# Performance work log

Measured on AMD Instinct MI355X. Metric: run time of the kernel, lower is better.

## Reference

```python
import jax, jax.numpy as jnp
import numpy as np

N_SRC = 50000
N_DST = 50000
N_EDGES = 1_600_000
D_IN = 128
D_OUT = 128
NUM_HEADS = 8
SCALE = float((D_OUT // NUM_HEADS) ** 0.5)


def setup_inputs() -> dict:
    key = jax.random.key(0)
    ks = jax.random.split(key, 10)
    s = 1.0 / np.sqrt(D_IN)
    return {
        "src_feat": jax.random.normal(ks[0], (N_SRC, D_IN), dtype=jnp.float32),
        "dst_feat": jax.random.normal(ks[1], (N_DST, D_OUT), dtype=jnp.float32),
        "src_idx": jax.random.randint(ks[2], (N_EDGES,), 0, N_SRC, dtype=jnp.int64),
        "dst_idx": jax.random.randint(ks[3], (N_EDGES,), 0, N_DST, dtype=jnp.int64),
        "Wq": jax.random.normal(ks[4], (D_OUT, D_OUT), dtype=jnp.float32) * s,
        "bq": jnp.zeros((D_OUT,), dtype=jnp.float32),
        "Wk": jax.random.normal(ks[5], (D_OUT, D_IN), dtype=jnp.float32) * s,
        "bk": jnp.zeros((D_OUT,), dtype=jnp.float32),
        "Wv": jax.random.normal(ks[6], (D_OUT, D_IN), dtype=jnp.float32) * s,
        "bv": jnp.zeros((D_OUT,), dtype=jnp.float32),
    }


def reference(src_feat, dst_feat, src_idx, dst_idx, Wq, bq, Wk, bk, Wv, bv):
    # Node-level projections (torch Linear: x @ W.T + b)
    Q = dst_feat @ Wq.T + bq            # [N_dst, D_OUT]
    K = src_feat @ Wk.T + bk            # [N_src, D_OUT]
    V = src_feat @ Wv.T + bv            # [N_src, D_OUT]

    # Edge-wise full-dim dot-product score (heads only affect the scale)
    score = jnp.sum(Q[dst_idx] * K[src_idx], axis=-1) / SCALE  # [E]

    # Segment softmax over incoming edges of each destination node
    m = jax.ops.segment_max(score, dst_idx, num_segments=N_DST)   # [N_dst]
    e = jnp.exp(score - m[dst_idx])                               # [E]
    denom = jax.ops.segment_sum(e, dst_idx, num_segments=N_DST)   # [N_dst]
    attn = e / denom[dst_idx]                                     # [E]

    # Weighted V scatter-sum to destination nodes
    out = jax.ops.segment_sum(attn[:, None] * V[src_idx], dst_idx,
                              num_segments=N_DST)                 # [N_dst, D_OUT]
    return out
```

## Files before the change

kernel.cpp:

```cpp
#include <hip/hip_runtime.h>
#include <hip/hip_bf16.h>


#define D 128
#define INV_SCALE 0.25f
#define E1 4096
#define BCAP 10240

typedef __attribute__((ext_vector_type(8))) short bf16x8;
typedef __attribute__((ext_vector_type(4))) float f32x4;
typedef __attribute__((ext_vector_type(4))) int v4i;
typedef __attribute__((ext_vector_type(4))) unsigned v4u;

static __device__ __forceinline__ unsigned short f2bf(float f) {
  unsigned u = __float_as_uint(f);
  u += 0x7fff + ((u >> 16) & 1);
  return (unsigned short)(u >> 16);
}
static __device__ __forceinline__ float bfl(unsigned u) {
  return __uint_as_float(u << 16);
}
static __device__ __forceinline__ float bfh(unsigned u) {
  return __uint_as_float(u & 0xffff0000u);
}

__global__ __launch_bounds__(256) void cvt_w_kernel(
    const float* __restrict__ Wq, const float* __restrict__ Wk,
    const float* __restrict__ Wv, unsigned short* __restrict__ oq,
    unsigned short* __restrict__ ok, unsigned short* __restrict__ ov, int n) {
  int i = blockIdx.x * 256 + threadIdx.x;
  if (i < n) {
    oq[i] = f2bf(Wq[i]);
    ok[i] = f2bf(Wk[i]);
    ov[i] = f2bf(Wv[i]);
  }
}

__global__ __launch_bounds__(256) void gemm_q_kernel(
    const float* __restrict__ X, const unsigned short* __restrict__ Wb,
    const float* __restrict__ bias, float* __restrict__ out, int N) {
  const int lane = threadIdx.x & 63;
  const int l15 = lane & 15, quad = lane >> 4;
  const int row0 = blockIdx.x * 64 + (threadIdx.x >> 6) * 16;

  f32x4 acc[8];
#pragma unroll
  for (int t = 0; t < 8; ++t) acc[t] = (f32x4){0.f, 0.f, 0.f, 0.f};

  int ar = row0 + l15;
  if (ar >= N) ar = N - 1;
  const float* ap = X + (size_t)ar * D + quad * 8;

#pragma unroll
  for (int kc = 0; kc < 4; ++kc) {
    float4 a0 = *(const float4*)(ap + kc * 32);
    float4 a1 = *(const float4*)(ap + kc * 32 + 4);
    bf16x8 a;
    a[0] = f2bf(a0.x); a[1] = f2bf(a0.y); a[2] = f2bf(a0.z); a[3] = f2bf(a0.w);
    a[4] = f2bf(a1.x); a[5] = f2bf(a1.y); a[6] = f2bf(a1.z); a[7] = f2bf(a1.w);
#pragma unroll
    for (int t = 0; t < 8; ++t) {
      bf16x8 b =
          *(const bf16x8*)(Wb + (size_t)(t * 16 + l15) * D + kc * 32 + quad * 8);
      acc[t] = __builtin_amdgcn_mfma_f32_16x16x32_bf16(a, b, acc[t], 0, 0, 0);
    }
  }
#pragma unroll
  for (int t = 0; t < 8; ++t) {
    const int c = t * 16 + l15;
    const float bc = bias[c];
#pragma unroll
    for (int r = 0; r < 4; ++r) {
      const int row = row0 + quad * 4 + r;
      if (row < N) out[(size_t)row * D + c] = acc[t][r] + bc;
    }
  }
}

__global__ __launch_bounds__(256) void gemm_kv_kernel(
    const float* __restrict__ X, const unsigned short* __restrict__ Wk,
    const float* __restrict__ bk, const unsigned short* __restrict__ Wv,
    const float* __restrict__ bv, unsigned short* __restrict__ KV, int N) {
  __shared__ unsigned short stage[64][256];
  const int tid = threadIdx.x;
  const int lane = tid & 63;
  const int l15 = lane & 15, quad = lane >> 4;
  const int wave = tid >> 6;
  const int row0 = blockIdx.x * 64 + wave * 16;

  f32x4 accK[8], accV[8];
#pragma unroll
  for (int t = 0; t < 8; ++t) {
    accK[t] = (f32x4){0.f, 0.f, 0.f, 0.f};
    accV[t] = (f32x4){0.f, 0.f, 0.f, 0.f};
  }

  int ar = row0 + l15;
  if (ar >= N) ar = N - 1;
  const float* ap = X + (size_t)ar * D + quad * 8;

#pragma unroll
  for (int kc = 0; kc < 4; ++kc) {
    float4 a0 = *(const float4*)(ap + kc * 32);
    float4 a1 = *(const float4*)(ap + kc * 32 + 4);
    bf16x8 a;
    a[0] = f2bf(a0.x); a[1] = f2bf(a0.y); a[2] = f2bf(a0.z); a[3] = f2bf(a0.w);
    a[4] = f2bf(a1.x); a[5] = f2bf(a1.y); a[6] = f2bf(a1.z); a[7] = f2bf(a1.w);
#pragma unroll
    for (int t = 0; t < 8; ++t) {
      const size_t boff = (size_t)(t * 16 + l15) * D + kc * 32 + quad * 8;
      bf16x8 b0 = *(const bf16x8*)(Wk + boff);
      bf16x8 b1 = *(const bf16x8*)(Wv + boff);
      accK[t] = __builtin_amdgcn_mfma_f32_16x16x32_bf16(a, b0, accK[t], 0, 0, 0);
      accV[t] = __builtin_amdgcn_mfma_f32_16x16x32_bf16(a, b1, accV[t], 0, 0, 0);
    }
  }
#pragma unroll
  for (int t = 0; t < 8; ++t) {
    const int c = t * 16 + l15;
    const float bkc = bk[c], bvc = bv[c];
    const int ki = ((c >> 2) << 3) + (c & 3);
#pragma unroll
    for (int r = 0; r < 4; ++r) {
      const int lr = wave * 16 + quad * 4 + r;
      stage[lr][ki] = f2bf(accK[t][r] + bkc);
      stage[lr][ki + 4] = f2bf(accV[t][r] + bvc);
    }
  }
  __syncthreads();
  const int row_base = blockIdx.x * 64;
#pragma unroll
  for (int i = 0; i < 8; ++i) {
    int idx = i * 256 + tid;
    int lr = idx >> 5;
    int c8 = (idx & 31) << 3;
    int grow = row_base + lr;
    if (grow < N)
      *(f32x4*)(KV + (size_t)grow * 256 + c8) = *(const f32x4*)&stage[lr][c8];
  }
}

__global__ __launch_bounds__(256) void bin1_kernel(
    const int* __restrict__ src_idx, const int* __restrict__ dst_idx,
    int* __restrict__ bins, int* __restrict__ bcount, int n) {
  __shared__ int h[256], basebuf[256], cur[256];
  const int tid = threadIdx.x;
  const int e0 = blockIdx.x * E1;
  int dv[16], sv[16];
#pragma unroll
  for (int i = 0; i < 4; ++i) {
    int e = e0 + i * 1024 + tid * 4;
    if (e + 3 < n) {
      v4i d4 = __builtin_nontemporal_load((const v4i*)(dst_idx + e));
      v4i s4 = __builtin_nontemporal_load((const v4i*)(src_idx + e));
      dv[4 * i + 0] = d4.x; dv[4 * i + 1] = d4.y;
      dv[4 * i + 2] = d4.z; dv[4 * i + 3] = d4.w;
      sv[4 * i + 0] = s4.x; sv[4 * i + 1] = s4.y;
      sv[4 * i + 2] = s4.z; sv[4 * i + 3] = s4.w;
    } else {
      for (int k = 0; k < 4; ++k) {
        int ee = e + k;
        dv[4 * i + k] = (ee < n) ? dst_idx[ee] : -1;
        sv[4 * i + k] = (ee < n) ? src_idx[ee] : 0;
      }
    }
  }
  h[tid] = 0;
  __syncthreads();
#pragma unroll
  for (int i = 0; i < 16; ++i)
    if (dv[i] >= 0) atomicAdd(&h[dv[i] >> 8], 1);
  __syncthreads();
  const int c = h[tid];
  if (c > 0) basebuf[tid] = tid * BCAP + atomicAdd(&bcount[tid], c);
  cur[tid] = 0;
  __syncthreads();
#pragma unroll
  for (int i = 0; i < 16; ++i) {
    if (dv[i] >= 0) {
      const int b = dv[i] >> 8;
      const int r = atomicAdd(&cur[b], 1);
      const int off = basebuf[b] + r;
      if (off < (b + 1) * BCAP)
        bins[off] = sv[i] | ((dv[i] & 255) << 17);
    }
  }
}

__global__ __launch_bounds__(256) void bin2_kernel(
    const int* __restrict__ bins, const int* __restrict__ bcount,
    int* __restrict__ csr, int* __restrict__ rowptr, int n_dst, int n_edges) {
  __shared__ int h[256], ofs[256], cur[256], red[256];
  const int tid = threadIdx.x;
  const int b = blockIdx.x;
  red[tid] = (tid < b) ? min(bcount[tid], BCAP) : 0;
  __syncthreads();
  for (int off = 128; off > 0; off >>= 1) {
    if (tid < off) red[tid] += red[tid + off];
    __syncthreads();
  }
  const int gbase = red[0];
  const int cnt = min(bcount[b], BCAP);
  h[tid] = 0;
  __syncthreads();
  const int* bb = bins + b * BCAP;
  for (int i = tid; i < cnt; i += 256) atomicAdd(&h[(bb[i] >> 17) & 255], 1);
  __syncthreads();
  const int myh = h[tid];
  red[tid] = myh;
  __syncthreads();
  for (int off = 1; off < 256; off <<= 1) {
    int t = (tid >= off) ? red[tid - off] : 0;
    __syncthreads();
    red[tid] += t;
    __syncthreads();
  }
  ofs[tid] = red[tid] - myh;
  cur[tid] = 0;
  const int d = b * 256 + tid;
  if (d < n_dst) rowptr[d] = gbase + ofs[tid];
  if (b == 0 && tid == 0) rowptr[n_dst] = n_edges;
  __syncthreads();
  for (int i = tid; i < cnt; i += 256) {
    const int p = bb[i];
    const int j = (p >> 17) & 255;
    const int r = atomicAdd(&cur[j], 1);
    csr[gbase + ofs[j] + r] = p & 0x1ffff;
  }
}

__global__ __launch_bounds__(256) void fused_agg_kernel(
    const float* __restrict__ Q, const unsigned short* __restrict__ KV,
    const int* __restrict__ csr, const int* __restrict__ rowptr,
    float* __restrict__ out, int n_dst) {
  const int lane = threadIdx.x & 63;
  const int half = lane >> 5;
  const int hl = lane & 31;
  int d = blockIdx.x * 4 + (threadIdx.x >> 6);
  if (d >= n_dst) return;
  d = __builtin_amdgcn_readfirstlane(d);
  const int start = __builtin_amdgcn_readfirstlane(rowptr[d]);
  const int n = __builtin_amdgcn_readfirstlane(rowptr[d + 1]) - start;

  float4 q = *(const float4*)(Q + (size_t)d * D + 4 * hl);
  q.x *= INV_SCALE; q.y *= INV_SCALE; q.z *= INV_SCALE; q.w *= INV_SCALE;

  float4 acc = make_float4(0.f, 0.f, 0.f, 0.f);
  float den = 0.f;

  for (int base = 0; base < n; base += 64) {
    const int il = base + lane;
    const int iv =
        __builtin_nontemporal_load(csr + start + ((il < n) ? il : (n - 1)));
    const int m = min(64, n - base);
    for (int j8 = 0; j8 < m; j8 += 8) {
      float pv[4];
      v4u kv[4];
      bool val[4];
#pragma unroll
      for (int u = 0; u < 4; ++u) {
        const int jj = j8 + 2 * u + half;
        val[u] = jj < m;
        const int s = __shfl(iv, jj, 64);
        kv[u] = *(const v4u*)(KV + (size_t)s * 256 + hl * 8);
        pv[u] = q.x * bfl(kv[u].x) + q.y * bfh(kv[u].x) + q.z * bfl(kv[u].y) +
                q.w * bfh(kv[u].y);
      }
#pragma unroll
      for (int u = 0; u < 4; ++u) {
        float p = pv[u];
#pragma unroll
        for (int msk = 16; msk > 0; msk >>= 1) p += __shfl_xor(p, msk, 64);
        const float e = val[u] ? __expf(p) : 0.f;
        acc.x += e * bfl(kv[u].z);
        acc.y += e * bfh(kv[u].z);
        acc.z += e * bfl(kv[u].w);
        acc.w += e * bfh(kv[u].w);
        den += e;
      }
    }
  }

  acc.x += __shfl_xor(acc.x, 32, 64);
  acc.y += __shfl_xor(acc.y, 32, 64);
  acc.z += __shfl_xor(acc.z, 32, 64);
  acc.w += __shfl_xor(acc.w, 32, 64);
  den += __shfl_xor(den, 32, 64);

  if (half == 0) {
    const float r = (n > 0) ? 1.0f / den : 0.f;
    f32x4 o = (f32x4){acc.x * r, acc.y * r, acc.z * r, acc.w * r};
    __builtin_nontemporal_store(o, (f32x4*)(out + (size_t)d * D + 4 * hl));
  }
}

extern "C" void kernel_launch(void* const* d_in, const int* in_sizes, int n_in,
                              void* d_out, int out_size, void* d_ws,
                              size_t ws_size, hipStream_t stream) {
  const float* src_feat = (const float*)d_in[0];
  const float* dst_feat = (const float*)d_in[1];
  const int* src_idx = (const int*)d_in[2];
  const int* dst_idx = (const int*)d_in[3];
  const float* Wq = (const float*)d_in[4];
  const float* bq = (const float*)d_in[5];
  const float* Wk = (const float*)d_in[6];
  const float* bk = (const float*)d_in[7];
  const float* Wv = (const float*)d_in[8];
  const float* bv = (const float*)d_in[9];

  const int n_src = in_sizes[0] / D;
  const int n_dst = in_sizes[1] / D;
  const int n_edges = in_sizes[2];
  const int nbk = (n_dst + 255) >> 8;

  float* out = (float*)d_out;

  float* Q = (float*)d_ws;
  unsigned short* KV = (unsigned short*)(Q + (size_t)n_dst * D);
  unsigned short* Wqb = KV + (size_t)n_src * 256;
  unsigned short* Wkb = Wqb + D * D;
  unsigned short* Wvb = Wkb + D * D;
  int* bcount = (int*)(Wvb + D * D);
  int* rowptr = bcount + 256;
  int* csr = rowptr + (n_dst + 1);
  int* bins = csr + n_edges;

  (void)hipMemsetAsync(bcount, 0, 256 * sizeof(int), stream);

  dim3 blk(256);

  cvt_w_kernel<<<dim3((D * D + 255) / 256), blk, 0, stream>>>(
      Wq, Wk, Wv, Wqb, Wkb, Wvb, D * D);
  gemm_q_kernel<<<dim3((n_dst + 63) / 64), blk, 0, stream>>>(dst_feat, Wqb, bq,
                                                             Q, n_dst);
  gemm_kv_kernel<<<dim3((n_src + 63) / 64), blk, 0, stream>>>(
      src_feat, Wkb, bk, Wvb, bv, KV, n_src);

  bin1_kernel<<<dim3((n_edges + E1 - 1) / E1), blk, 0, stream>>>(
      src_idx, dst_idx, bins, bcount, n_edges);
  bin2_kernel<<<dim3(nbk), blk, 0, stream>>>(bins, bcount, csr, rowptr, n_dst,
                                             n_edges);

  fused_agg_kernel<<<dim3((n_dst + 3) / 4), blk, 0, stream>>>(Q, KV, csr,
                                                              rowptr, out,
                                                              n_dst);
}
```

Measured before the change: 313.4 us.

## Merge preprocessing kernels by block range and rework aggregation wave mapping

The weight conversion and first binning pass now share one launch, and the second binning pass, Q GEMM and KV GEMM share another, with each block choosing its role from its block index. This cuts the launch count from five to two and lets independent stages run concurrently. The aggregation kernel now has each 16-lane group handle one edge with two 16-byte loads per edge, and processes eight edges per iteration. The dot-product reduction uses DPP adds over 16 lanes instead of 32-lane shuffles, and exp is replaced by exp2 with log2e folded into the Q scale. The merged kernels mix different shared-memory and register needs in one launch, which could lower occupancy for the lighter roles.

```diff
diff --git a/kernel.cpp b/kernel.cpp
--- a/kernel.cpp
+++ b/kernel.cpp
@@ -3,9 +3,9 @@
 
 
 #define D 128
-#define INV_SCALE 0.25f
 #define E1 4096
 #define BCAP 10240
+#define LOG2E 1.44269504088896340736f
 
 typedef __attribute__((ext_vector_type(8))) short bf16x8;
 typedef __attribute__((ext_vector_type(4))) float f32x4;
@@ -24,11 +24,18 @@
   return __uint_as_float(u & 0xffff0000u);
 }
 
-__global__ __launch_bounds__(256) void cvt_w_kernel(
-    const float* __restrict__ Wq, const float* __restrict__ Wk,
+template <int CTRL>
+static __device__ __forceinline__ float dpp_add(float x) {
+  int y = __builtin_amdgcn_update_dpp(0, __float_as_int(x), CTRL, 0xF, 0xF, false);
+  return x + __int_as_float(y);
+}
+
+
+static __device__ __forceinline__ void cvt_w_body(
+    int bx, const float* __restrict__ Wq, const float* __restrict__ Wk,
     const float* __restrict__ Wv, unsigned short* __restrict__ oq,
     unsigned short* __restrict__ ok, unsigned short* __restrict__ ov, int n) {
-  int i = blockIdx.x * 256 + threadIdx.x;
+  int i = bx * 256 + threadIdx.x;
   if (i < n) {
     oq[i] = f2bf(Wq[i]);
     ok[i] = f2bf(Wk[i]);
@@ -36,116 +43,12 @@
   }
 }
 
-__global__ __launch_bounds__(256) void gemm_q_kernel(
-    const float* __restrict__ X, const unsigned short* __restrict__ Wb,
-    const float* __restrict__ bias, float* __restrict__ out, int N) {
-  const int lane = threadIdx.x & 63;
-  const int l15 = lane & 15, quad = lane >> 4;
-  const int row0 = blockIdx.x * 64 + (threadIdx.x >> 6) * 16;
-
-  f32x4 acc[8];
-#pragma unroll
-  for (int t = 0; t < 8; ++t) acc[t] = (f32x4){0.f, 0.f, 0.f, 0.f};
-
-  int ar = row0 + l15;
-  if (ar >= N) ar = N - 1;
-  const float* ap = X + (size_t)ar * D + quad * 8;
-
-#pragma unroll
-  for (int kc = 0; kc < 4; ++kc) {
-    float4 a0 = *(const float4*)(ap + kc * 32);
-    float4 a1 = *(const float4*)(ap + kc * 32 + 4);
-    bf16x8 a;
-    a[0] = f2bf(a0.x); a[1] = f2bf(a0.y); a[2] = f2bf(a0.z); a[3] = f2bf(a0.w);
-    a[4] = f2bf(a1.x); a[5] = f2bf(a1.y); a[6] = f2bf(a1.z); a[7] = f2bf(a1.w);
-#pragma unroll
-    for (int t = 0; t < 8; ++t) {
-      bf16x8 b =
-          *(const bf16x8*)(Wb + (size_t)(t * 16 + l15) * D + kc * 32 + quad * 8);
-      acc[t] = __builtin_amdgcn_mfma_f32_16x16x32_bf16(a, b, acc[t], 0, 0, 0);
-    }
-  }
-#pragma unroll
-  for (int t = 0; t < 8; ++t) {
-    const int c = t * 16 + l15;
-    const float bc = bias[c];
-#pragma unroll
-    for (int r = 0; r < 4; ++r) {
-      const int row = row0 + quad * 4 + r;
-      if (row < N) out[(size_t)row * D + c] = acc[t][r] + bc;
-    }
-  }
-}
-
-__global__ __launch_bounds__(256) void gemm_kv_kernel(
-    const float* __restrict__ X, const unsigned short* __restrict__ Wk,
-    const float* __restrict__ bk, const unsigned short* __restrict__ Wv,
-    const float* __restrict__ bv, unsigned short* __restrict__ KV, int N) {
-  __shared__ unsigned short stage[64][256];
+static __device__ void bin1_body(
+    int bx, int* h, int* basebuf, int* cur, const int* __restrict__ src_idx,
+    const int* __restrict__ dst_idx, int* __restrict__ bins,
+    int* __restrict__ bcount, int n) {
   const int tid = threadIdx.x;
-  const int lane = tid & 63;
-  const int l15 = lane & 15, quad = lane >> 4;
-  const int wave = tid >> 6;
-  const int row0 = blockIdx.x * 64 + wave * 16;
-
-  f32x4 accK[8], accV[8];
-#pragma unroll
-  for (int t = 0; t < 8; ++t) {
-    accK[t] = (f32x4){0.f, 0.f, 0.f, 0.f};
-    accV[t] = (f32x4){0.f, 0.f, 0.f, 0.f};
-  }
-
-  int ar = row0 + l15;
-  if (ar >= N) ar = N - 1;
-  const float* ap = X + (size_t)ar * D + quad * 8;
-
-#pragma unroll
-  for (int kc = 0; kc < 4; ++kc) {
-    float4 a0 = *(const float4*)(ap + kc * 32);
-    float4 a1 = *(const float4*)(ap + kc * 32 + 4);
-    bf16x8 a;
-    a[0] = f2bf(a0.x); a[1] = f2bf(a0.y); a[2] = f2bf(a0.z); a[3] = f2bf(a0.w);
-    a[4] = f2bf(a1.x); a[5] = f2bf(a1.y); a[6] = f2bf(a1.z); a[7] = f2bf(a1.w);
-#pragma unroll
-    for (int t = 0; t < 8; ++t) {
-      const size_t boff = (size_t)(t * 16 + l15) * D + kc * 32 + quad * 8;
-      bf16x8 b0 = *(const bf16x8*)(Wk + boff);
-      bf16x8 b1 = *(const bf16x8*)(Wv + boff);
-      accK[t] = __builtin_amdgcn_mfma_f32_16x16x32_bf16(a, b0, accK[t], 0, 0, 0);
-      accV[t] = __builtin_amdgcn_mfma_f32_16x16x32_bf16(a, b1, accV[t], 0, 0, 0);
-    }
-  }
-#pragma unroll
-  for (int t = 0; t < 8; ++t) {
-    const int c = t * 16 + l15;
-    const float bkc = bk[c], bvc = bv[c];
-    const int ki = ((c >> 2) << 3) + (c & 3);
-#pragma unroll
-    for (int r = 0; r < 4; ++r) {
-      const int lr = wave * 16 + quad * 4 + r;
-      stage[lr][ki] = f2bf(accK[t][r] + bkc);
-      stage[lr][ki + 4] = f2bf(accV[t][r] + bvc);
-    }
-  }
-  __syncthreads();
-  const int row_base = blockIdx.x * 64;
-#pragma unroll
-  for (int i = 0; i < 8; ++i) {
-    int idx = i * 256 + tid;
-    int lr = idx >> 5;
-    int c8 = (idx & 31) << 3;
-    int grow = row_base + lr;
-    if (grow < N)
-      *(f32x4*)(KV + (size_t)grow * 256 + c8) = *(const f32x4*)&stage[lr][c8];
-  }
-}
-
-__global__ __launch_bounds__(256) void bin1_kernel(
-    const int* __restrict__ src_idx, const int* __restrict__ dst_idx,
-    int* __restrict__ bins, int* __restrict__ bcount, int n) {
-  __shared__ int h[256], basebuf[256], cur[256];
-  const int tid = threadIdx.x;
-  const int e0 = blockIdx.x * E1;
+  const int e0 = bx * E1;
   int dv[16], sv[16];
 #pragma unroll
   for (int i = 0; i < 4; ++i) {
@@ -187,12 +90,15 @@
   }
 }
 
-__global__ __launch_bounds__(256) void bin2_kernel(
-    const int* __restrict__ bins, const int* __restrict__ bcount,
-    int* __restrict__ csr, int* __restrict__ rowptr, int n_dst, int n_edges) {
-  __shared__ int h[256], ofs[256], cur[256], red[256];
+static __device__ void bin2_body(
+    int b, int* smem, const int* __restrict__ bins,
+    const int* __restrict__ bcount, int* __restrict__ csr,
+    int* __restrict__ rowptr, int n_dst, int n_edges) {
+  int* h = smem;
+  int* ofs = smem + 256;
+  int* cur = smem + 512;
+  int* red = smem + 768;
   const int tid = threadIdx.x;
-  const int b = blockIdx.x;
   red[tid] = (tid < b) ? min(bcount[tid], BCAP) : 0;
   __syncthreads();
   for (int off = 128; off > 0; off >>= 1) {
@@ -229,68 +135,231 @@
   }
 }
 
+static __device__ void gemm_q_body(
+    int bx, const float* __restrict__ X, const unsigned short* __restrict__ Wb,
+    const float* __restrict__ bias, float* __restrict__ out, int N) {
+  const int lane = threadIdx.x & 63;
+  const int l15 = lane & 15, quad = lane >> 4;
+  const int row0 = bx * 64 + (threadIdx.x >> 6) * 16;
+
+  f32x4 acc[8];
+#pragma unroll
+  for (int t = 0; t < 8; ++t) acc[t] = (f32x4){0.f, 0.f, 0.f, 0.f};
+
+  int ar = row0 + l15;
+  if (ar >= N) ar = N - 1;
+  const float* ap = X + (size_t)ar * D + quad * 8;
+
+#pragma unroll
+  for (int kc = 0; kc < 4; ++kc) {
+    float4 a0 = *(const float4*)(ap + kc * 32);
+    float4 a1 = *(const float4*)(ap + kc * 32 + 4);
+    bf16x8 a;
+    a[0] = f2bf(a0.x); a[1] = f2bf(a0.y); a[2] = f2bf(a0.z); a[3] = f2bf(a0.w);
+    a[4] = f2bf(a1.x); a[5] = f2bf(a1.y); a[6] = f2bf(a1.z); a[7] = f2bf(a1.w);
+#pragma unroll
+    for (int t = 0; t < 8; ++t) {
+      bf16x8 b =
+          *(const bf16x8*)(Wb + (size_t)(t * 16 + l15) * D + kc * 32 + quad * 8);
+      acc[t] = __builtin_amdgcn_mfma_f32_16x16x32_bf16(a, b, acc[t], 0, 0, 0);
+    }
+  }
+#pragma unroll
+  for (int t = 0; t < 8; ++t) {
+    const int c = t * 16 + l15;
+    const float bc = bias[c];
+#pragma unroll
+    for (int r = 0; r < 4; ++r) {
+      const int row = row0 + quad * 4 + r;
+      if (row < N) out[(size_t)row * D + c] = acc[t][r] + bc;
+    }
+  }
+}
+
+static __device__ void gemm_kv_body(
+    int bx, unsigned short (*stage)[256], const float* __restrict__ X,
+    const unsigned short* __restrict__ Wk, const float* __restrict__ bk,
+    const unsigned short* __restrict__ Wv, const float* __restrict__ bv,
+    unsigned short* __restrict__ KV, int N) {
+  const int tid = threadIdx.x;
+  const int lane = tid & 63;
+  const int l15 = lane & 15, quad = lane >> 4;
+  const int wave = tid >> 6;
+  const int row0 = bx * 64 + wave * 16;
+
+  f32x4 accK[8], accV[8];
+#pragma unroll
+  for (int t = 0; t < 8; ++t) {
+    accK[t] = (f32x4){0.f, 0.f, 0.f, 0.f};
+    accV[t] = (f32x4){0.f, 0.f, 0.f, 0.f};
+  }
+
+  int ar = row0 + l15;
+  if (ar >= N) ar = N - 1;
+  const float* ap = X + (size_t)ar * D + quad * 8;
+
+#pragma unroll
+  for (int kc = 0; kc < 4; ++kc) {
+    float4 a0 = *(const float4*)(ap + kc * 32);
+    float4 a1 = *(const float4*)(ap + kc * 32 + 4);
+    bf16x8 a;
+    a[0] = f2bf(a0.x); a[1] = f2bf(a0.y); a[2] = f2bf(a0.z); a[3] = f2bf(a0.w);
+    a[4] = f2bf(a1.x); a[5] = f2bf(a1.y); a[6] = f2bf(a1.z); a[7] = f2bf(a1.w);
+#pragma unroll
+    for (int t = 0; t < 8; ++t) {
+      const size_t boff = (size_t)(t * 16 + l15) * D + kc * 32 + quad * 8;
+      bf16x8 b0 = *(const bf16x8*)(Wk + boff);
+      bf16x8 b1 = *(const bf16x8*)(Wv + boff);
+      accK[t] = __builtin_amdgcn_mfma_f32_16x16x32_bf16(a, b0, accK[t], 0, 0, 0);
+      accV[t] = __builtin_amdgcn_mfma_f32_16x16x32_bf16(a, b1, accV[t], 0, 0, 0);
+    }
+  }
+#pragma unroll
+  for (int t = 0; t < 8; ++t) {
+    const int c = t * 16 + l15;
+    const float bkc = bk[c], bvc = bv[c];
+    const int ki = ((c >> 2) << 3) + (c & 3);
+#pragma unroll
+    for (int r = 0; r < 4; ++r) {
+      const int lr = wave * 16 + quad * 4 + r;
+      stage[lr][ki] = f2bf(accK[t][r] + bkc);
+      stage[lr][ki + 4] = f2bf(accV[t][r] + bvc);
+    }
+  }
+  __syncthreads();
+  const int row_base = bx * 64;
+#pragma unroll
+  for (int i = 0; i < 8; ++i) {
+    int idx = i * 256 + tid;
+    int lr = idx >> 5;
+    int c8 = (idx & 31) << 3;
+    int grow = row_base + lr;
+    if (grow < N)
+      *(f32x4*)(KV + (size_t)grow * 256 + c8) = *(const f32x4*)&stage[lr][c8];
+  }
+}
+
+
+__global__ __launch_bounds__(256) void front_kernel(
+    const float* __restrict__ Wq, const float* __restrict__ Wk,
+    const float* __restrict__ Wv, unsigned short* __restrict__ oq,
+    unsigned short* __restrict__ ok, unsigned short* __restrict__ ov, int nw,
+    const int* __restrict__ src_idx, const int* __restrict__ dst_idx,
+    int* __restrict__ bins, int* __restrict__ bcount, int n_edges, int gcvt) {
+  __shared__ int sh[768];
+  const int b = blockIdx.x;
+  if (b < gcvt) {
+    cvt_w_body(b, Wq, Wk, Wv, oq, ok, ov, nw);
+  } else {
+    bin1_body(b - gcvt, sh, sh + 256, sh + 512, src_idx, dst_idx, bins, bcount,
+              n_edges);
+  }
+}
+
+__global__ __launch_bounds__(256) void mid_kernel(
+    const float* __restrict__ dst_feat, const unsigned short* __restrict__ Wqb,
+    const float* __restrict__ bq, float* __restrict__ Q, int n_dst,
+    const float* __restrict__ src_feat, const unsigned short* __restrict__ Wkb,
+    const float* __restrict__ bk, const unsigned short* __restrict__ Wvb,
+    const float* __restrict__ bv, unsigned short* __restrict__ KV, int n_src,
+    const int* __restrict__ bins, const int* __restrict__ bcount,
+    int* __restrict__ csr, int* __restrict__ rowptr, int n_edges, int nbk,
+    int gq) {
+  __shared__ unsigned short stage[64][256];
+  const int b = blockIdx.x;
+  if (b < nbk) {
+    bin2_body(b, (int*)stage, bins, bcount, csr, rowptr, n_dst, n_edges);
+  } else if (b < nbk + gq) {
+    gemm_q_body(b - nbk, dst_feat, Wqb, bq, Q, n_dst);
+  } else {
+    gemm_kv_body(b - nbk - gq, stage, src_feat, Wkb, bk, Wvb, bv, KV, n_src);
+  }
+}
+
 __global__ __launch_bounds__(256) void fused_agg_kernel(
     const float* __restrict__ Q, const unsigned short* __restrict__ KV,
     const int* __restrict__ csr, const int* __restrict__ rowptr,
     float* __restrict__ out, int n_dst) {
   const int lane = threadIdx.x & 63;
-  const int half = lane >> 5;
-  const int hl = lane & 31;
+  const int g = lane >> 4;
+  const int gl = lane & 15;
   int d = blockIdx.x * 4 + (threadIdx.x >> 6);
   if (d >= n_dst) return;
   d = __builtin_amdgcn_readfirstlane(d);
   const int start = __builtin_amdgcn_readfirstlane(rowptr[d]);
   const int n = __builtin_amdgcn_readfirstlane(rowptr[d + 1]) - start;
 
-  float4 q = *(const float4*)(Q + (size_t)d * D + 4 * hl);
-  q.x *= INV_SCALE; q.y *= INV_SCALE; q.z *= INV_SCALE; q.w *= INV_SCALE;
-
-  float4 acc = make_float4(0.f, 0.f, 0.f, 0.f);
+  const float qs = 0.25f * LOG2E;
+  float4 q0 = *(const float4*)(Q + (size_t)d * D + 4 * gl);
+  float4 q1 = *(const float4*)(Q + (size_t)d * D + 64 + 4 * gl);
+  q0.x *= qs; q0.y *= qs; q0.z *= qs; q0.w *= qs;
+  q1.x *= qs; q1.y *= qs; q1.z *= qs; q1.w *= qs;
+
+  f32x4 acc0 = (f32x4){0.f, 0.f, 0.f, 0.f};
+  f32x4 acc1 = (f32x4){0.f, 0.f, 0.f, 0.f};
   float den = 0.f;
+  const int* cp = csr + start;
 
   for (int base = 0; base < n; base += 64) {
     const int il = base + lane;
-    const int iv =
-        __builtin_nontemporal_load(csr + start + ((il < n) ? il : (n - 1)));
+    const int iv = __builtin_nontemporal_load(cp + ((il < n) ? il : (n - 1)));
     const int m = min(64, n - base);
-    for (int j8 = 0; j8 < m; j8 += 8) {
-      float pv[4];
-      v4u kv[4];
-      bool val[4];
-#pragma unroll
-      for (int u = 0; u < 4; ++u) {
-        const int jj = j8 + 2 * u + half;
-        val[u] = jj < m;
-        const int s = __shfl(iv, jj, 64);
-        kv[u] = *(const v4u*)(KV + (size_t)s * 256 + hl * 8);
-        pv[u] = q.x * bfl(kv[u].x) + q.y * bfh(kv[u].x) + q.z * bfl(kv[u].y) +
-                q.w * bfh(kv[u].y);
-      }
-#pragma unroll
-      for (int u = 0; u < 4; ++u) {
-        float p = pv[u];
-#pragma unroll
-        for (int msk = 16; msk > 0; msk >>= 1) p += __shfl_xor(p, msk, 64);
-        const float e = val[u] ? __expf(p) : 0.f;
-        acc.x += e * bfl(kv[u].z);
-        acc.y += e * bfh(kv[u].z);
-        acc.z += e * bfl(kv[u].w);
-        acc.w += e * bfh(kv[u].w);
-        den += e;
-      }
-    }
-  }
-
-  acc.x += __shfl_xor(acc.x, 32, 64);
-  acc.y += __shfl_xor(acc.y, 32, 64);
-  acc.z += __shfl_xor(acc.z, 32, 64);
-  acc.w += __shfl_xor(acc.w, 32, 64);
-  den += __shfl_xor(den, 32, 64);
-
-  if (half == 0) {
+    for (int j = 0; j < m; j += 8) {
+      const int j0 = j + g, j1 = j + 4 + g;
+      const int s0 = __shfl(iv, j0, 64);
+      const int s1 = __shfl(iv, j1, 64);
+      const unsigned short* r0 = KV + (size_t)s0 * 256 + gl * 8;
+      const unsigned short* r1 = KV + (size_t)s1 * 256 + gl * 8;
+      const v4u a0 = *(const v4u*)(r0);
+      const v4u a1 = *(const v4u*)(r0 + 128);
+      const v4u b0 = *(const v4u*)(r1);
+      const v4u b1 = *(const v4u*)(r1 + 128);
+      float p0 = (q0.x * bfl(a0.x) + q0.y * bfh(a0.x) + q0.z * bfl(a0.y) +
+                  q0.w * bfh(a0.y)) +
+                 (q1.x * bfl(a1.x) + q1.y * bfh(a1.x) + q1.z * bfl(a1.y) +
+                  q1.w * bfh(a1.y));
+      float p1 = (q0.x * bfl(b0.x) + q0.y * bfh(b0.x) + q0.z * bfl(b0.y) +
+                  q0.w * bfh(b0.y)) +
+                 (q1.x * bfl(b1.x) + q1.y * bfh(b1.x) + q1.z * bfl(b1.y) +
+                  q1.w * bfh(b1.y));
+      p0 = dpp_add<0xB1>(p0);  p1 = dpp_add<0xB1>(p1);
+      p0 = dpp_add<0x4E>(p0);  p1 = dpp_add<0x4E>(p1);
+      p0 = dpp_add<0x141>(p0); p1 = dpp_add<0x141>(p1);
+      p0 = dpp_add<0x140>(p0); p1 = dpp_add<0x140>(p1);
+      const float e0 = (j0 < m) ? exp2f(p0) : 0.f;
+      const float e1 = (j1 < m) ? exp2f(p1) : 0.f;
+      acc0[0] += e0 * bfl(a0.z); acc0[1] += e0 * bfh(a0.z);
+      acc0[2] += e0 * bfl(a0.w); acc0[3] += e0 * bfh(a0.w);
+      acc1[0] += e0 * bfl(a1.z); acc1[1] += e0 * bfh(a1.z);
+      acc1[2] += e0 * bfl(a1.w); acc1[3] += e0 * bfh(a1.w);
+      acc0[0] += e1 * bfl(b0.z); acc0[1] += e1 * bfh(b0.z);
+      acc0[2] += e1 * bfl(b0.w); acc0[3] += e1 * bfh(b0.w);
+      acc1[0] += e1 * bfl(b1.z); acc1[1] += e1 * bfh(b1.z);
+      acc1[2] += e1 * bfl(b1.w); acc1[3] += e1 * bfh(b1.w);
+      den += e0 + e1;
+    }
+  }
+
+#pragma unroll
+  for (int msk = 16; msk <= 32; msk <<= 1) {
+    acc0[0] += __shfl_xor(acc0[0], msk, 64);
+    acc0[1] += __shfl_xor(acc0[1], msk, 64);
+    acc0[2] += __shfl_xor(acc0[2], msk, 64);
+    acc0[3] += __shfl_xor(acc0[3], msk, 64);
+    acc1[0] += __shfl_xor(acc1[0], msk, 64);
+    acc1[1] += __shfl_xor(acc1[1], msk, 64);
+    acc1[2] += __shfl_xor(acc1[2], msk, 64);
+    acc1[3] += __shfl_xor(acc1[3], msk, 64);
+    den += __shfl_xor(den, msk, 64);
+  }
+
+  if (lane < 16) {
     const float r = (n > 0) ? 1.0f / den : 0.f;
-    f32x4 o = (f32x4){acc.x * r, acc.y * r, acc.z * r, acc.w * r};
-    __builtin_nontemporal_store(o, (f32x4*)(out + (size_t)d * D + 4 * hl));
+    f32x4 o0 = (f32x4){acc0[0] * r, acc0[1] * r, acc0[2] * r, acc0[3] * r};
+    f32x4 o1 = (f32x4){acc1[0] * r, acc1[1] * r, acc1[2] * r, acc1[3] * r};
+    __builtin_nontemporal_store(o0, (f32x4*)(out + (size_t)d * D + 4 * gl));
+    __builtin_nontemporal_store(o1,
+                                (f32x4*)(out + (size_t)d * D + 64 + 4 * gl));
   }
 }
 
@@ -328,18 +397,18 @@
   (void)hipMemsetAsync(bcount, 0, 256 * sizeof(int), stream);
 
   dim3 blk(256);
-
-  cvt_w_kernel<<<dim3((D * D + 255) / 256), blk, 0, stream>>>(
-      Wq, Wk, Wv, Wqb, Wkb, Wvb, D * D);
-  gemm_q_kernel<<<dim3((n_dst + 63) / 64), blk, 0, stream>>>(dst_feat, Wqb, bq,
-                                                             Q, n_dst);
-  gemm_kv_kernel<<<dim3((n_src + 63) / 64), blk, 0, stream>>>(
-      src_feat, Wkb, bk, Wvb, bv, KV, n_src);
-
-  bin1_kernel<<<dim3((n_edges + E1 - 1) / E1), blk, 0, stream>>>(
-      src_idx, dst_idx, bins, bcount, n_edges);
-  bin2_kernel<<<dim3(nbk), blk, 0, stream>>>(bins, bcount, csr, rowptr, n_dst,
-                                             n_edges);
+  const int gcvt = (D * D + 255) / 256;
+  const int g1 = (n_edges + E1 - 1) / E1;
+  const int gq = (n_dst + 63) / 64;
+  const int gkv = (n_src + 63) / 64;
+
+  front_kernel<<<dim3(gcvt + g1), blk, 0, stream>>>(
+      Wq, Wk, Wv, Wqb, Wkb, Wvb, D * D, src_idx, dst_idx, bins, bcount,
+      n_edges, gcvt);
+
+  mid_kernel<<<dim3(nbk + gq + gkv), blk, 0, stream>>>(
+      dst_feat, Wqb, bq, Q, n_dst, src_feat, Wkb, bk, Wvb, bv, KV, n_src, bins,
+      bcount, csr, rowptr, n_edges, nbk, gq);
 
   fused_agg_kernel<<<dim3((n_dst + 3) / 4), blk, 0, stream>>>(Q, KV, csr,
                                                               rowptr, out,
```

New measurement: 292.4 us. 6.7% less time.
